# Performance work log

Hardware: AMD Instinct MI355X
Metric: run time of the kernel (lower is better)

## Reference

```python
import jax, jax.numpy as jnp
import numpy as np

K_PROPOSALS = 16  # Marsaglia-Tsang acceptance rate > 0.95 for alpha > 1/3; P(all 16 rejected) < 1e-20

B, D_IN, H, L = 32768, 1024, 512, 64


def _glorot(key, shape):
    fan_in, fan_out = shape
    return jax.random.normal(key, shape, jnp.float32) * jnp.sqrt(2.0 / (fan_in + fan_out))


def setup_inputs() -> dict:
    key = jax.random.key(0)
    ks = jax.random.split(key, 4)
    return {
        "x": jax.random.normal(ks[0], (B, D_IN), jnp.float32),
        "W0": _glorot(ks[1], (D_IN, H)),
        "b0": jnp.zeros((H,), jnp.float32),
        "W1": _glorot(ks[2], (H, H)),
        "b1": jnp.zeros((H,), jnp.float32),
        "Wl": _glorot(ks[3], (H, L)),
        "bl": jnp.zeros((L,), jnp.float32),
    }


def _marsaglia_tsang_sample(alpha):
    """Vectorized Marsaglia-Tsang gamma(alpha, 1) rejection sampler.
    Draws K_PROPOSALS candidates per element and selects the first accepted one
    (equivalent to the original per-element while-loop, flattened for SIMD)."""
    d = alpha - 1.0 / 3.0                     # [B, L]
    c = 1.0 / jnp.sqrt(9.0 * d)               # [B, L]
    kz, ku = jax.random.split(jax.random.key(1))
    z = jax.random.normal(kz, (K_PROPOSALS,) + alpha.shape, alpha.dtype)   # [K, B, L]
    u = jax.random.uniform(ku, (K_PROPOSALS,) + alpha.shape, alpha.dtype,
                           minval=1e-7, maxval=1.0)                        # [K, B, L]
    v = (1.0 + c * z) ** 3                    # [K, B, L]
    pos = v > 0.0                             # equivalent to z > -1/c (= b1)
    safe_v = jnp.where(pos, v, 1.0)
    # accept iff z > b1 AND log(u) <= b2 (negation of the resampling condition)
    b2 = 0.5 * jnp.square(z) + d - d * safe_v + d * jnp.log(safe_v)
    accept = pos & (jnp.log(u) < b2)          # [K, B, L]
    first = jnp.argmax(accept, axis=0)        # index of first accepted proposal
    samples = d * safe_v                      # [K, B, L]
    return jnp.take_along_axis(samples, first[None], axis=0)[0]  # [B, L]


def reference(x, W0, b0, W1, b1, Wl, bl):
    # dense encoder: two ReLU hidden layers + linear latent head producing alpha
    h = jax.nn.relu(x @ W0 + b0)
    h = jax.nn.relu(h @ W1 + b1)
    # softplus + 0.5 keeps alpha > 1/3 so d > 0 (required by Marsaglia-Tsang)
    alpha = jax.nn.softplus(h @ Wl + bl) + 0.5
    sample = _marsaglia_tsang_sample(alpha)
    return alpha, sample
```

## Files before the change

kernel.cpp:

```cpp
#include <hip/hip_runtime.h>
#include <cstdint>
#include <cstddef>

typedef __attribute__((ext_vector_type(8))) short short8;
typedef __attribute__((ext_vector_type(4))) float floatx4;

constexpr int MDIM = 32768;
constexpr int DIN  = 1024;
constexpr int HDIM = 512;
constexpr int LDIM = 64;
constexpr uint32_t BL = (uint32_t)MDIM * (uint32_t)LDIM;

__host__ __device__ __forceinline__ void tf2x32(uint32_t k0, uint32_t k1,
                                                uint32_t x0, uint32_t x1,
                                                uint32_t& o0, uint32_t& o1) {
  const uint32_t k2 = k0 ^ k1 ^ 0x1BD11BDAu;
  x0 += k0; x1 += k1;
#define TFR(r) { x0 += x1; x1 = (x1 << (r)) | (x1 >> (32 - (r))); x1 ^= x0; }
  TFR(13) TFR(15) TFR(26) TFR(6)
  x0 += k1; x1 += k2 + 1u;
  TFR(17) TFR(29) TFR(16) TFR(24)
  x0 += k2; x1 += k0 + 2u;
  TFR(13) TFR(15) TFR(26) TFR(6)
  x0 += k0; x1 += k1 + 3u;
  TFR(17) TFR(29) TFR(16) TFR(24)
  x0 += k1; x1 += k2 + 4u;
  TFR(13) TFR(15) TFR(26) TFR(6)
  x0 += k2; x1 += k0 + 5u;
#undef TFR
  o0 = x0; o1 = x1;
}

__device__ __forceinline__ uint32_t tf_bits(uint32_t k0, uint32_t k1, uint32_t j) {
  uint32_t o0, o1;
  tf2x32(k0, k1, 0u, j, o0, o1);
  return o0 ^ o1;
}

__device__ __forceinline__ float b2f(unsigned short s) {
  return __uint_as_float((uint32_t)s << 16);
}
__device__ __forceinline__ unsigned short f2b(float f) {
  uint32_t u = __float_as_uint(f);
  u += 0x7fffu + ((u >> 16) & 1u);
  return (unsigned short)(u >> 16);
}
__device__ __forceinline__ void split3(float x, unsigned short& h,
                                       unsigned short& l, unsigned short& l2) {
  h = f2b(x);
  const float r = __fsub_rn(x, b2f(h));
  l = f2b(r);
  const float r2 = __fsub_rn(r, b2f(l));
  l2 = f2b(r2);
}

__device__ __forceinline__ float erfinv_f32(float x) {
  const float xx = __fmul_rn(x, x);
  float w = -log1pf(-xx);
  float p;
  if (w < 5.0f) {
    w = __fadd_rn(w, -2.5f);
    p = 2.81022636e-08f;
    p = __fadd_rn(__fmul_rn(p, w), 3.43273939e-07f);
    p = __fadd_rn(__fmul_rn(p, w), -3.5233877e-06f);
    p = __fadd_rn(__fmul_rn(p, w), -4.39150654e-06f);
    p = __fadd_rn(__fmul_rn(p, w), 0.00021858087f);
    p = __fadd_rn(__fmul_rn(p, w), -0.00125372503f);
    p = __fadd_rn(__fmul_rn(p, w), -0.00417768164f);
    p = __fadd_rn(__fmul_rn(p, w), 0.246640727f);
    p = __fadd_rn(__fmul_rn(p, w), 1.50140941f);
  } else {
    w = __fadd_rn(sqrtf(w), -3.0f);
    p = -0.000200214257f;
    p = __fadd_rn(__fmul_rn(p, w), 0.000100950558f);
    p = __fadd_rn(__fmul_rn(p, w), 0.00134934322f);
    p = __fadd_rn(__fmul_rn(p, w), -0.00367342844f);
    p = __fadd_rn(__fmul_rn(p, w), 0.00573950773f);
    p = __fadd_rn(__fmul_rn(p, w), -0.0076224613f);
    p = __fadd_rn(__fmul_rn(p, w), 0.00943887047f);
    p = __fadd_rn(__fmul_rn(p, w), 1.00167406f);
    p = __fadd_rn(__fmul_rn(p, w), 2.83297682f);
  }
  return __fmul_rn(p, x);
}

#define LO_N  (-0x1.fffffep-1f)
#define DIFF_N (2.0f)
#define SQRT2_F ((float)1.4142135623730951)
#define DIFF_U (0x1.fffffcp-1f)
#define MINV_U (1e-7f)
#define THIRD_F ((float)(1.0 / 3.0))

__device__ __forceinline__ float gamma_draw(float d, float c, uint32_t j,
                                            uint32_t kz0, uint32_t kz1,
                                            uint32_t ku0, uint32_t ku1,
                                            bool& accept) {
  const uint32_t zb = tf_bits(kz0, kz1, j);
  const uint32_t ub = tf_bits(ku0, ku1, j);
  const float fz = __fsub_rn(__uint_as_float((zb >> 9) | 0x3f800000u), 1.0f);
  float un = __fadd_rn(__fmul_rn(fz, DIFF_N), LO_N);
  un = fmaxf(un, LO_N);
  const float z = __fmul_rn(SQRT2_F, erfinv_f32(un));
  const float fu = __fsub_rn(__uint_as_float((ub >> 9) | 0x3f800000u), 1.0f);
  float uu = __fadd_rn(__fmul_rn(fu, DIFF_U), MINV_U);
  uu = fmaxf(uu, MINV_U);
  const float t1 = __fadd_rn(1.0f, __fmul_rn(c, z));
  const float v = __fmul_rn(t1, __fmul_rn(t1, t1));
  const bool pos = (v > 0.0f);
  const float sv = pos ? v : 1.0f;
  const float b2 = __fadd_rn(
      __fsub_rn(__fadd_rn(__fmul_rn(0.5f, __fmul_rn(z, z)), d),
                __fmul_rn(d, sv)),
      __fmul_rn(d, logf(sv)));
  const float lu = logf(uu);
  accept = pos && (lu < b2);
  return __fmul_rn(d, sv);
}

__global__ __launch_bounds__(256) void split_transpose(
    const float* __restrict__ W, unsigned short* __restrict__ D, int K, int N) {
  __shared__ unsigned short th[32][33], tl[32][33], tl2[32][33];
  const int t = threadIdx.x;
  const int nb = N / 32;
  const int k0 = (blockIdx.x / nb) * 32, n0 = (blockIdx.x % nb) * 32;
#pragma unroll
  for (int i = 0; i < 4; ++i) {
    const int e = i * 256 + t;
    const int kk = e >> 5, nn = e & 31;
    const float x = W[(size_t)(k0 + kk) * N + (n0 + nn)];
    split3(x, th[kk][nn], tl[kk][nn], tl2[kk][nn]);
  }
  __syncthreads();
  const size_t PL = (size_t)N * K;
#pragma unroll
  for (int i = 0; i < 4; ++i) {
    const int e = i * 256 + t;
    const int nn = e >> 5, kk = e & 31;
    const size_t o = (size_t)(n0 + nn) * K + (k0 + kk);
    D[o] = th[kk][nn];
    D[PL + o] = tl[kk][nn];
    D[2 * PL + o] = tl2[kk][nn];
  }
}

template <int K>
__global__ __launch_bounds__(256) void gemm_split_mfma(
    const float* __restrict__ A, const unsigned short* __restrict__ BT,
    const float* __restrict__ bias, float* __restrict__ C) {
  constexpr int N = 512;
  constexpr size_t PL = (size_t)N * K;
  __shared__ unsigned short As[3][128 * 32];
  __shared__ unsigned short Bs[3][128 * 32];
  const int t = threadIdx.x;
  const int lane = t & 63, w = t >> 6;
  const int wm = w >> 1, wn = w & 1;
  const int ln = lane & 15, kq = lane >> 4;
  const int b = blockIdx.x;
  const int xcd = b & 7, slot = b >> 3;
  const int bm = (xcd * 32 + (slot >> 2)) * 128;
  const int bn = (slot & 3) * 128;

  floatx4 acc[4][4];
#pragma unroll
  for (int i = 0; i < 4; ++i)
#pragma unroll
    for (int j = 0; j < 4; ++j) acc[i][j] = (floatx4)0.0f;

  for (int k0 = 0; k0 < K; k0 += 32) {
#pragma unroll
    for (int p = 0; p < 3; ++p)
#pragma unroll
      for (int i = 0; i < 2; ++i) {
        const int e = w * 1024 + i * 512 + lane * 8;
        const int n = e >> 5, kc = e & 31;
        const unsigned short* g = BT + p * PL + (size_t)(bn + n) * K + (k0 + kc);
        __builtin_amdgcn_global_load_lds(
            (const __attribute__((address_space(1))) unsigned int*)g,
            (__attribute__((address_space(3))) unsigned int*)&Bs[p][w * 1024 + i * 512],
            16, 0, 0);
      }
#pragma unroll
    for (int it = 0; it < 4; ++it) {
      const int e4 = (it * 256 + t) * 4;
      const int m = e4 >> 5, kc = e4 & 31;
      const float4 q = *reinterpret_cast<const float4*>(
          &A[(size_t)(bm + m) * K + (k0 + kc)]);
      ushort4 h, l, l2;
      split3(q.x, h.x, l.x, l2.x);
      split3(q.y, h.y, l.y, l2.y);
      split3(q.z, h.z, l.z, l2.z);
      split3(q.w, h.w, l.w, l2.w);
      *reinterpret_cast<ushort4*>(&As[0][m * 32 + kc]) = h;
      *reinterpret_cast<ushort4*>(&As[1][m * 32 + kc]) = l;
      *reinterpret_cast<ushort4*>(&As[2][m * 32 + kc]) = l2;
    }
    __syncthreads();
    short8 af[3][4], bf[3][4];
#pragma unroll
    for (int mi = 0; mi < 4; ++mi)
#pragma unroll
      for (int p = 0; p < 3; ++p)
        af[p][mi] = *reinterpret_cast<const short8*>(
            &As[p][(wm * 64 + mi * 16 + ln) * 32 + kq * 8]);
#pragma unroll
    for (int ni = 0; ni < 4; ++ni)
#pragma unroll
      for (int p = 0; p < 3; ++p)
        bf[p][ni] = *reinterpret_cast<const short8*>(
            &Bs[p][(wn * 64 + ni * 16 + ln) * 32 + kq * 8]);
#pragma unroll
    for (int mi = 0; mi < 4; ++mi)
#pragma unroll
      for (int ni = 0; ni < 4; ++ni) {
        floatx4 a = acc[mi][ni];
        a = __builtin_amdgcn_mfma_f32_16x16x32_bf16(af[0][mi], bf[0][ni], a, 0, 0, 0);
        a = __builtin_amdgcn_mfma_f32_16x16x32_bf16(af[0][mi], bf[1][ni], a, 0, 0, 0);
        a = __builtin_amdgcn_mfma_f32_16x16x32_bf16(af[1][mi], bf[0][ni], a, 0, 0, 0);
        a = __builtin_amdgcn_mfma_f32_16x16x32_bf16(af[1][mi], bf[1][ni], a, 0, 0, 0);
        a = __builtin_amdgcn_mfma_f32_16x16x32_bf16(af[0][mi], bf[2][ni], a, 0, 0, 0);
        a = __builtin_amdgcn_mfma_f32_16x16x32_bf16(af[2][mi], bf[0][ni], a, 0, 0, 0);
        acc[mi][ni] = a;
      }
    __syncthreads();
  }
#pragma unroll
  for (int ni = 0; ni < 4; ++ni) {
    const int n = bn + wn * 64 + ni * 16 + ln;
    const float bb = bias[n];
#pragma unroll
    for (int mi = 0; mi < 4; ++mi)
#pragma unroll
      for (int r = 0; r < 4; ++r) {
        const int m = bm + wm * 64 + mi * 16 + kq * 4 + r;
        C[(size_t)m * N + n] = fmaxf(__fadd_rn(acc[mi][ni][r], bb), 0.0f);
      }
  }
}

__global__ __launch_bounds__(256) void gemm3_sampler(
    const float* __restrict__ A, const float* __restrict__ Wl,
    const float* __restrict__ bl, float* __restrict__ out,
    uint32_t kz0, uint32_t kz1, uint32_t ku0, uint32_t ku1) {
  constexpr int BM = 64, BK = 16, K = 512, N = 64;
  constexpr int LDA = BM + 4, LDB = N + 4;
  __shared__ float Ash[BK * LDA];
  __shared__ float Bsh[BK * LDB];
  __shared__ float alphaS[BM * N];
  __shared__ unsigned short queue[BM * N];
  __shared__ int nrej;
  const int t = threadIdx.x;
  const int tx = t % 16, ty = t / 16;
  const int bm = blockIdx.x * BM;
  if (t == 0) nrej = 0;
  float acc[4][4] = {};
  const int aRow = t / 4, aCol = (t % 4) * 4;
  const int bRow = t / 16, bCol = (t % 16) * 4;

  for (int k0 = 0; k0 < K; k0 += BK) {
    {
      const float4 q = *reinterpret_cast<const float4*>(
          A + (size_t)(bm + aRow) * K + (k0 + aCol));
      Ash[(aCol + 0) * LDA + aRow] = q.x;
      Ash[(aCol + 1) * LDA + aRow] = q.y;
      Ash[(aCol + 2) * LDA + aRow] = q.z;
      Ash[(aCol + 3) * LDA + aRow] = q.w;
    }
    {
      const float4 q = *reinterpret_cast<const float4*>(
          Wl + (size_t)(k0 + bRow) * N + bCol);
      *reinterpret_cast<float4*>(&Bsh[bRow * LDB + bCol]) = q;
    }
    __syncthreads();
#pragma unroll
    for (int k = 0; k < BK; ++k) {
      float a[4], b[4];
#pragma unroll
      for (int i = 0; i < 4; ++i) a[i] = Ash[k * LDA + ty * 4 + i];
#pragma unroll
      for (int j = 0; j < 4; ++j) b[j] = Bsh[k * LDB + tx * 4 + j];
#pragma unroll
      for (int i = 0; i < 4; ++i)
#pragma unroll
        for (int j = 0; j < 4; ++j) acc[i][j] = fmaf(a[i], b[j], acc[i][j]);
    }
    __syncthreads();
  }

  float bv[4];
#pragma unroll
  for (int j = 0; j < 4; ++j) bv[j] = bl[tx * 4 + j];

#pragma unroll 1
  for (int i = 0; i < 4; ++i) {
    const int row = bm + ty * 4 + i;
    float av[4], sv4[4];
    unsigned short rejloc[4];
    int nrl = 0;
#pragma unroll 1
    for (int j = 0; j < 4; ++j) {
      const float x = __fadd_rn(acc[i][j], bv[j]);
      const float sp = __fadd_rn(fmaxf(x, 0.0f), log1pf(expf(-fabsf(x))));
      const float alpha = __fadd_rn(sp, 0.5f);
      const int le = (ty * 4 + i) * 64 + tx * 4 + j;
      alphaS[le] = alpha;
      const float d = __fsub_rn(alpha, THIRD_F);
      const float c = __fdiv_rn(1.0f, sqrtf(__fmul_rn(9.0f, d)));
      bool acc0;
      const float s0 = gamma_draw(d, c, (uint32_t)row * 64u + (uint32_t)(tx * 4 + j),
                                  kz0, kz1, ku0, ku1, acc0);
      av[j] = alpha;
      sv4[j] = s0;
      if (!acc0) rejloc[nrl++] = (unsigned short)le;
    }
    if (nrl) {
      const int base = atomicAdd(&nrej, nrl);
      for (int q = 0; q < nrl; ++q) queue[base + q] = rejloc[q];
    }
    *reinterpret_cast<float4*>(&out[(size_t)row * 64 + tx * 4]) =
        *reinterpret_cast<float4*>(av);
    *reinterpret_cast<float4*>(&out[(size_t)BL + (size_t)row * 64 + tx * 4]) =
        *reinterpret_cast<float4*>(sv4);
  }
  __syncthreads();

  const int n = nrej;
  for (int q = t; q < n; q += 256) {
    const int le = queue[q];
    const float alpha = alphaS[le];
    const float d = __fsub_rn(alpha, THIRD_F);
    const float c = __fdiv_rn(1.0f, sqrtf(__fmul_rn(9.0f, d)));
    const uint32_t e = (uint32_t)bm * 64u + (uint32_t)le;
#pragma unroll 1
    for (int k = 1; k < 16; ++k) {
      bool acck;
      const float s = gamma_draw(d, c, (uint32_t)k * BL + e,
                                 kz0, kz1, ku0, ku1, acck);
      if (acck) {
        out[(size_t)BL + e] = s;
        break;
      }
    }
  }
}

extern "C" void kernel_launch(void* const* d_in, const int* in_sizes, int n_in,
                              void* d_out, int out_size, void* d_ws, size_t ws_size,
                              hipStream_t stream) {
  (void)in_sizes; (void)n_in; (void)out_size; (void)ws_size;
  const float* x  = (const float*)d_in[0];
  const float* W0 = (const float*)d_in[1];
  const float* b0 = (const float*)d_in[2];
  const float* W1 = (const float*)d_in[3];
  const float* b1 = (const float*)d_in[4];
  const float* Wl = (const float*)d_in[5];
  const float* bl = (const float*)d_in[6];
  float* h1 = (float*)d_ws;
  float* h2 = h1 + (size_t)MDIM * HDIM;
  float* out = (float*)d_out;

  unsigned short* W0T = (unsigned short*)out;
  unsigned short* W1T = (unsigned short*)(out + BL);

  uint32_t kz0, kz1, ku0, ku1;
  tf2x32(0u, 1u, 0u, 0u, kz0, kz1);
  tf2x32(0u, 1u, 0u, 1u, ku0, ku1);

  split_transpose<<<dim3((DIN / 32) * (HDIM / 32)), 256, 0, stream>>>(
      W0, W0T, DIN, HDIM);
  split_transpose<<<dim3((HDIM / 32) * (HDIM / 32)), 256, 0, stream>>>(
      W1, W1T, HDIM, HDIM);

  gemm_split_mfma<DIN><<<dim3(1024), 256, 0, stream>>>(x, W0T, b0, h1);
  gemm_split_mfma<HDIM><<<dim3(1024), 256, 0, stream>>>(h1, W1T, b1, h2);
  gemm3_sampler<<<dim3(MDIM / 64), 256, 0, stream>>>(h2, Wl, bl, out,
                                                     kz0, kz1, ku0, ku1);
}
```

Measured before the change: 587.5 us.

## Use plain 2D grid for GEMMs and unroll sampler epilogue with bitmask rejection queue

The GEMM kernels drop the XCD-aware block swizzle and use a straightforward 2D grid, with the x index over N tiles and the y index over M tiles. The sampler epilogue is fully unrolled: it computes all 16 alpha/sample values into registers, records rejections in a bitmask, then writes the outputs and pushes rejected indices to the shared queue. The goal is more instruction-level parallelism in the transcendental-heavy sampler. In exchange it loses the explicit L2 locality per XCD in the GEMMs and raises register pressure in the sampler.

```diff
diff --git a/kernel.cpp b/kernel.cpp
--- a/kernel.cpp
+++ b/kernel.cpp
@@ -155,10 +155,7 @@
   const int lane = t & 63, w = t >> 6;
   const int wm = w >> 1, wn = w & 1;
   const int ln = lane & 15, kq = lane >> 4;
-  const int b = blockIdx.x;
-  const int xcd = b & 7, slot = b >> 3;
-  const int bm = (xcd * 32 + (slot >> 2)) * 128;
-  const int bn = (slot & 3) * 128;
+  const int bm = blockIdx.y * 128, bn = blockIdx.x * 128;
 
   floatx4 acc[4][4];
 #pragma unroll
@@ -290,36 +287,44 @@
 #pragma unroll
   for (int j = 0; j < 4; ++j) bv[j] = bl[tx * 4 + j];
 
-#pragma unroll 1
-  for (int i = 0; i < 4; ++i) {
-    const int row = bm + ty * 4 + i;
-    float av[4], sv4[4];
-    unsigned short rejloc[4];
-    int nrl = 0;
-#pragma unroll 1
+  float alpha_r[16], s0_r[16];
+  uint32_t rejmask = 0;
+#pragma unroll
+  for (int i = 0; i < 4; ++i)
+#pragma unroll
     for (int j = 0; j < 4; ++j) {
+      const int idx = i * 4 + j;
       const float x = __fadd_rn(acc[i][j], bv[j]);
       const float sp = __fadd_rn(fmaxf(x, 0.0f), log1pf(expf(-fabsf(x))));
       const float alpha = __fadd_rn(sp, 0.5f);
-      const int le = (ty * 4 + i) * 64 + tx * 4 + j;
-      alphaS[le] = alpha;
       const float d = __fsub_rn(alpha, THIRD_F);
       const float c = __fdiv_rn(1.0f, sqrtf(__fmul_rn(9.0f, d)));
+      const uint32_t e = (uint32_t)(bm + ty * 4 + i) * 64u
+                         + (uint32_t)(tx * 4 + j);
       bool acc0;
-      const float s0 = gamma_draw(d, c, (uint32_t)row * 64u + (uint32_t)(tx * 4 + j),
-                                  kz0, kz1, ku0, ku1, acc0);
-      av[j] = alpha;
-      sv4[j] = s0;
-      if (!acc0) rejloc[nrl++] = (unsigned short)le;
-    }
-    if (nrl) {
-      const int base = atomicAdd(&nrej, nrl);
-      for (int q = 0; q < nrl; ++q) queue[base + q] = rejloc[q];
-    }
-    *reinterpret_cast<float4*>(&out[(size_t)row * 64 + tx * 4]) =
-        *reinterpret_cast<float4*>(av);
-    *reinterpret_cast<float4*>(&out[(size_t)BL + (size_t)row * 64 + tx * 4]) =
-        *reinterpret_cast<float4*>(sv4);
+      const float s0 = gamma_draw(d, c, e, kz0, kz1, ku0, ku1, acc0);
+      alpha_r[idx] = alpha;
+      s0_r[idx] = s0;
+      alphaS[(ty * 4 + i) * 64 + tx * 4 + j] = alpha;
+      rejmask |= (acc0 ? 0u : (1u << idx));
+    }
+#pragma unroll
+  for (int i = 0; i < 4; ++i) {
+    const int row = bm + ty * 4 + i;
+    float4 av = { alpha_r[i * 4 + 0], alpha_r[i * 4 + 1],
+                  alpha_r[i * 4 + 2], alpha_r[i * 4 + 3] };
+    float4 sv = { s0_r[i * 4 + 0], s0_r[i * 4 + 1],
+                  s0_r[i * 4 + 2], s0_r[i * 4 + 3] };
+    *reinterpret_cast<float4*>(&out[(size_t)row * 64 + tx * 4]) = av;
+    *reinterpret_cast<float4*>(&out[(size_t)BL + (size_t)row * 64 + tx * 4]) = sv;
+  }
+  while (rejmask) {
+    const int idx = __ffs(rejmask) - 1;
+    rejmask &= rejmask - 1;
+    const int i = idx >> 2, j = idx & 3;
+    const int le = (ty * 4 + i) * 64 + tx * 4 + j;
+    const int base = atomicAdd(&nrej, 1);
+    queue[base] = (unsigned short)le;
   }
   __syncthreads();
 
@@ -370,8 +375,9 @@
   split_transpose<<<dim3((HDIM / 32) * (HDIM / 32)), 256, 0, stream>>>(
       W1, W1T, HDIM, HDIM);
 
-  gemm_split_mfma<DIN><<<dim3(1024), 256, 0, stream>>>(x, W0T, b0, h1);
-  gemm_split_mfma<HDIM><<<dim3(1024), 256, 0, stream>>>(h1, W1T, b1, h2);
+  dim3 g12(HDIM / 128, MDIM / 128);
+  gemm_split_mfma<DIN><<<g12, 256, 0, stream>>>(x, W0T, b0, h1);
+  gemm_split_mfma<HDIM><<<g12, 256, 0, stream>>>(h1, W1T, b1, h2);
   gemm3_sampler<<<dim3(MDIM / 64), 256, 0, stream>>>(h2, Wl, bl, out,
                                                      kz0, kz1, ku0, ku1);
 }
```

Result: faster. 571.8 us (-2.7%).
